# Kernel optimization log

Hardware: AMD Instinct MI355X
Metric: run time of the kernel (lower is better)

Reference implementation:

```python
import jax, jax.numpy as jnp
import numpy as np

DIM = 128
POS_HID = 64
ATT_HID = DIM * 2
B, N = 4, 512


def _linear_init(key, fan_in, fan_out):
    # mimic torch Linear default init scale: U(-1/sqrt(fan_in), 1/sqrt(fan_in))
    kw, kb = jax.random.split(key)
    bound = 1.0 / np.sqrt(fan_in)
    W = jax.random.uniform(kw, (fan_in, fan_out), minval=-bound, maxval=bound, dtype=jnp.float32)
    b = jax.random.uniform(kb, (fan_out,), minval=-bound, maxval=bound, dtype=jnp.float32)
    return W, b


def setup_inputs() -> dict:
    key = jax.random.key(0)
    ks = jax.random.split(key, 6)
    x = jax.random.normal(ks[0], (B, DIM, N), dtype=jnp.float32)
    pos = jax.random.normal(ks[1], (B, N, 3), dtype=jnp.float32)
    Wqkv, bqkv = _linear_init(ks[2], DIM, DIM * 3)
    pW1, pb1 = _linear_init(ks[3], 3, POS_HID)
    pW2, pb2 = _linear_init(ks[4], POS_HID, DIM)
    k5a, k5b = jax.random.split(ks[5])
    aW1, ab1 = _linear_init(k5a, DIM, ATT_HID)
    aW2, ab2 = _linear_init(k5b, ATT_HID, DIM)
    return {"x": x, "pos": pos, "Wqkv": Wqkv, "bqkv": bqkv,
            "pW1": pW1, "pb1": pb1, "pW2": pW2, "pb2": pb2,
            "aW1": aW1, "ab1": ab1, "aW2": aW2, "ab2": ab2}


def reference(x, pos, Wqkv, bqkv, pW1, pb1, pW2, pb2, aW1, ab1, aW2, ab2):
    # x: [b, d, n] -> [b, n, d]
    xt = jnp.transpose(x, (0, 2, 1))
    qkv = xt @ Wqkv + bqkv                      # [b, n, 3d]
    q, k, v = jnp.split(qkv, 3, axis=-1)        # each [b, n, d]

    # pairwise relative positions: [b, i, j, 3]
    rel_pos = pos[:, :, None, :] - pos[:, None, :, :]
    # pos_mlp: Linear(3, hid) -> ReLU -> Linear(hid, d)
    rel_pos_emb = jax.nn.relu(rel_pos @ pW1 + pb1) @ pW2 + pb2   # [b, i, j, d]

    qk_rel = q[:, :, None, :] - k[:, None, :, :]                 # [b, i, j, d]
    v_ij = v[:, None, :, :] + rel_pos_emb                        # [b, i, j, d]

    # attn_mlp: Linear(d, 2d) -> ReLU -> Linear(2d, d)
    sim = jax.nn.relu((qk_rel + rel_pos_emb) @ aW1 + ab1) @ aW2 + ab2  # [b, i, j, d]
    attn = jax.nn.softmax(sim, axis=2)                           # softmax over j (dim=-2)
    agg = jnp.sum(attn * v_ij, axis=2)                           # [b, i, d]
    return jnp.transpose(agg, (0, 2, 1))                         # [b, d, n]
```

## Files before the change

kernel.cpp:

```cpp
#include <hip/hip_runtime.h>
#include <hip/hip_bf16.h>

#define B_ 4
#define N_ 512
#define D_ 128
#define LOG2E 1.4426950408889634f

typedef __attribute__((ext_vector_type(8))) short bf16x8;
typedef __attribute__((ext_vector_type(4))) short s16x4;
typedef __attribute__((ext_vector_type(4))) float f32x4;
typedef __attribute__((ext_vector_type(16))) float f32x16;

__device__ __forceinline__ f32x4 mfma16(bf16x8 a, bf16x8 b, f32x4 c) {
    return __builtin_amdgcn_mfma_f32_16x16x32_bf16(a, b, c, 0, 0, 0);
}
__device__ __forceinline__ f32x16 mfma32(bf16x8 a, bf16x8 b, f32x16 c) {
    return __builtin_amdgcn_mfma_f32_32x32x16_bf16(a, b, c, 0, 0, 0);
}
__device__ __forceinline__ short bf16b(float x) {
    __hip_bfloat16 h = __float2bfloat16(x);
    return *reinterpret_cast<short*>(&h);
}
__device__ __forceinline__ float b2f(short s) {
    unsigned u = ((unsigned)(unsigned short)s) << 16;
    union { unsigned u; float f; } c; c.u = u; return c.f;
}

__global__ void prep_misc_kernel(const float* __restrict__ aW1, const float* __restrict__ aW2,
                                 const float* __restrict__ pW2, const float* __restrict__ pb2,
                                 const float* __restrict__ ab1, const float* __restrict__ pos,
                                 const float* __restrict__ pW1, const float* __restrict__ x,
                                 const float* __restrict__ Wqkv, const float* __restrict__ bqkv,
                                 __hip_bfloat16* __restrict__ aW2T, __hip_bfloat16* __restrict__ pW2T,
                                 __hip_bfloat16* __restrict__ W12T, float* __restrict__ cvec,
                                 float* __restrict__ posw,
                                 float* __restrict__ q, float* __restrict__ k,
                                 short* __restrict__ vb_t) {
    const int bid = blockIdx.x;
    const int tid = threadIdx.x;
    if (bid < 128) {
        int idx = bid * 256 + tid;
        {
            int n = idx >> 8, k2 = idx & 255;
            aW2T[idx] = __float2bfloat16(aW2[k2 * 128 + n] * LOG2E);
        }
        if (idx < 128 * 64) {
            int n = idx >> 6, k2 = idx & 63;
            pW2T[idx] = __float2bfloat16(pW2[k2 * 128 + n]);
        }
        if (idx < 256 * 64) {
            int n = idx >> 6, h = idx & 63;
            float s = 0.f;
#pragma unroll 8
            for (int d = 0; d < 128; ++d) s += pW2[h * 128 + d] * aW1[d * 256 + n];
            W12T[idx] = __float2bfloat16(s);
        }
        if (idx < 256) {
            float s = ab1[idx];
#pragma unroll 8
            for (int d = 0; d < 128; ++d) s += pb2[d] * aW1[d * 256 + idx];
            cvec[idx] = s;
        }
    } else if (bid < 256) {
        int i4 = (bid - 128) * 256 + tid;
        int t = i4 >> 4, h4 = (i4 & 15) * 4;
        float p0 = pos[t * 3 + 0], p1 = pos[t * 3 + 1], p2 = pos[t * 3 + 2];
#pragma unroll
        for (int e = 0; e < 4; ++e) {
            int h = h4 + e;
            posw[t * 64 + h] = p0 * pW1[h] + p1 * pW1[64 + h] + p2 * pW1[128 + h];
        }
    } else {
        int idx = (bid - 256) * 256 + tid;
        int m = idx % 384;
        int g = idx / 384;
        int bn0 = g * 16;
        int b = bn0 >> 9, n0 = bn0 & (N_ - 1);
        const float* xp = x + (b * D_) * N_ + n0;
        float bias = bqkv[m];
        float acc[16];
#pragma unroll
        for (int t = 0; t < 16; ++t) acc[t] = bias;
#pragma unroll 2
        for (int d = 0; d < D_; ++d) {
            float wv = Wqkv[d * 384 + m];
            const float* xr = xp + d * N_;
            float4 x0 = *(const float4*)(xr);
            float4 x1 = *(const float4*)(xr + 4);
            float4 x2 = *(const float4*)(xr + 8);
            float4 x3 = *(const float4*)(xr + 12);
            acc[0]  = fmaf(x0.x, wv, acc[0]);  acc[1]  = fmaf(x0.y, wv, acc[1]);
            acc[2]  = fmaf(x0.z, wv, acc[2]);  acc[3]  = fmaf(x0.w, wv, acc[3]);
            acc[4]  = fmaf(x1.x, wv, acc[4]);  acc[5]  = fmaf(x1.y, wv, acc[5]);
            acc[6]  = fmaf(x1.z, wv, acc[6]);  acc[7]  = fmaf(x1.w, wv, acc[7]);
            acc[8]  = fmaf(x2.x, wv, acc[8]);  acc[9]  = fmaf(x2.y, wv, acc[9]);
            acc[10] = fmaf(x2.z, wv, acc[10]); acc[11] = fmaf(x2.w, wv, acc[11]);
            acc[12] = fmaf(x3.x, wv, acc[12]); acc[13] = fmaf(x3.y, wv, acc[13]);
            acc[14] = fmaf(x3.z, wv, acc[14]); acc[15] = fmaf(x3.w, wv, acc[15]);
        }
        if (m < 256) {
            float* dst = (m < 128) ? q : k;
            int mm = m & 127;
#pragma unroll
            for (int t = 0; t < 16; ++t)
                dst[(bn0 + t) * D_ + mm] = acc[t];
        } else {
            int d = m & 127;
            int jt = n0 >> 6;
            int jr = n0 & 63;
            int rtv = jr >> 5;
            int jrr0 = jr & 31;
            int ct = d >> 5;
            int lbase = d & 31;
            size_t tilebase = (size_t)b * 65536 + (size_t)jt * 8192
                            + (size_t)((rtv * 4 + ct) * 64) * 16;
#pragma unroll
            for (int tt = 0; tt < 4; ++tt) {
                int jrr = jrr0 + tt * 4;
                int rb = 4 * (jrr >> 3);
                int hi = (jrr >> 2) & 1;
                s16x4 pk;
                pk[0] = bf16b(acc[tt * 4 + 0]); pk[1] = bf16b(acc[tt * 4 + 1]);
                pk[2] = bf16b(acc[tt * 4 + 2]); pk[3] = bf16b(acc[tt * 4 + 3]);
                *(s16x4*)(vb_t + tilebase + (size_t)(lbase + 32 * hi) * 16 + rb) = pk;
            }
        }
    }
}

__global__ void qka_kernel(const float* __restrict__ q, const float* __restrict__ k,
                           const float* __restrict__ aW1,
                           float* __restrict__ qa, short* __restrict__ kab_t) {
    int col = threadIdx.x;
    int bn0 = blockIdx.x * 8;
    int b = bn0 >> 9, n0 = bn0 & (N_ - 1);
    const float* qp = q + (size_t)bn0 * D_;
    const float* kp = k + (size_t)bn0 * D_;
    float aq[8], ak[8];
#pragma unroll
    for (int t = 0; t < 8; ++t) { aq[t] = 0.f; ak[t] = 0.f; }
#pragma unroll 2
    for (int d = 0; d < D_; ++d) {
        float wv = aW1[d * 256 + col];
#pragma unroll
        for (int t = 0; t < 8; ++t) {
            aq[t] = fmaf(qp[t * D_ + d], wv, aq[t]);
            ak[t] = fmaf(kp[t * D_ + d], wv, ak[t]);
        }
    }
#pragma unroll
    for (int t = 0; t < 8; ++t)
        qa[(size_t)(bn0 + t) * 256 + col] = aq[t];
    int jt = n0 >> 6;
    int mt = (n0 >> 4) & 3;
    int lg0 = (n0 >> 2) & 3;
    int w = col >> 5, nt = (col >> 4) & 1, lc = col & 15;
#pragma unroll
    for (int half = 0; half < 2; ++half) {
        int lg = lg0 + half;
        int l = lg * 16 + lc;
        s16x4 pk;
        pk[0] = bf16b(ak[half * 4 + 0]); pk[1] = bf16b(ak[half * 4 + 1]);
        pk[2] = bf16b(ak[half * 4 + 2]); pk[3] = bf16b(ak[half * 4 + 3]);
        size_t base = (((((size_t)b * 8 + jt) * 8 + w) * 2 + nt) * 4 + mt) * 256 + l * 4;
        *(s16x4*)(kab_t + base) = pk;
    }
}

__global__ __launch_bounds__(512, 2) void fused_attn_kernel(
    const float* __restrict__ qa, const short* __restrict__ kab_t,
    const short* __restrict__ vb_t,
    const float* __restrict__ posw, const float* __restrict__ pb1,
    const __hip_bfloat16* __restrict__ pW2T, const float* __restrict__ pb2,
    const __hip_bfloat16* __restrict__ W12T, const float* __restrict__ cvec,
    const __hip_bfloat16* __restrict__ aW2T, const float* __restrict__ ab2,
    float* __restrict__ out)
{
    __shared__ __hip_bfloat16 ph_s[2][64][72];
    __shared__ __hip_bfloat16 hid_s[2][64][264];
    __shared__ float pwi_s[2][64];
    __shared__ float mrg_s[2][4][32][4];

    const int tid = threadIdx.x;
    const int w   = tid >> 6;
    const int l   = tid & 63;
    const int lg  = l >> 4;
    const int lc  = l & 15;
    const int l31 = l & 31;
    const int hi  = l >> 5;
    const int rt  = w >> 2;
    const int ct  = w & 3;
    const int gx8 = ((l31 >> 2) & 3) << 3;

    const int blk = (blockIdx.x & 7) * 128 + (blockIdx.x >> 3);
    const int b   = blk >> 8;
    const int i0  = (blk & 255) * 2;

    if (tid < 128) {
        int ii = tid >> 6, h = tid & 63;
        pwi_s[ii][h] = posw[(size_t)(b * N_ + i0 + ii) * 64 + h] + pb1[h];
    }

    const int col0  = 32 * w + lc;
    const int dcol2 = 32 * ct + l31;

    const float qr00 = qa[(b * N_ + i0) * 256 + col0] + cvec[col0];
    const float qr01 = qa[(b * N_ + i0) * 256 + col0 + 16] + cvec[col0 + 16];
    const float qr10 = qa[(b * N_ + i0 + 1) * 256 + col0] + cvec[col0];
    const float qr11 = qa[(b * N_ + i0 + 1) * 256 + col0 + 16] + cvec[col0 + 16];
    const float ab2_r = ab2[dcol2] * LOG2E;
    const float pb2_r = pb2[dcol2];

    const __hip_bfloat16* a2base = aW2T + (size_t)dcol2 * 256 + 8 * hi;
    bf16x8 bw2[16];
#pragma unroll
    for (int ks = 0; ks < 16; ++ks)
        bw2[ks] = *(const bf16x8*)(a2base + 16 * ks);
    const __hip_bfloat16* ppb = pW2T + (size_t)dcol2 * 64 + 8 * hi;
    const __hip_bfloat16* p12b = W12T + (size_t)(32 * w + lc) * 64 + 8 * lg;

    float m_run[2] = {-1e30f, -1e30f};
    float l_run[2] = {0.f, 0.f};
    float o_run[2] = {0.f, 0.f};
    float vv[2][16];

    const short* ktp0 = kab_t + (size_t)b * 131072 + w * 2048 + l * 4;
    const short* vtp0 = vb_t + (size_t)b * 65536 + ((rt * 4 + ct) * 64 + l) * 16;

    const int jl = tid >> 3;
    const int hb = (tid & 7) * 8;

    s16x4 vb4[4], kv[2][4];
#pragma unroll
    for (int q4 = 0; q4 < 4; ++q4)
        vb4[q4] = *(const s16x4*)(vtp0 + 4 * q4);
#pragma unroll
    for (int nt = 0; nt < 2; ++nt)
#pragma unroll
        for (int mt = 0; mt < 4; ++mt)
            kv[nt][mt] = *(const s16x4*)(ktp0 + nt * 1024 + mt * 256);
    __syncthreads();

    for (int jt = 0; jt < 8; ++jt) {
        bf16x8 bwp[4], bw12[2][2];
#pragma unroll
        for (int ks = 0; ks < 4; ++ks)
            bwp[ks] = *(const bf16x8*)(ppb + 16 * ks);
#pragma unroll
        for (int nt = 0; nt < 2; ++nt)
#pragma unroll
            for (int k2 = 0; k2 < 2; ++k2)
                bw12[nt][k2] = *(const bf16x8*)(p12b + nt * 1024 + k2 * 32);

        {
            const float* pj = posw + (size_t)(b * N_ + jt * 64 + jl) * 64 + hb;
            float4 x0 = *(const float4*)pj;
            float4 x1 = *(const float4*)(pj + 4);
            float xr[8] = {x0.x, x0.y, x0.z, x0.w, x1.x, x1.y, x1.z, x1.w};
#pragma unroll
            for (int ii = 0; ii < 2; ++ii) {
                bf16x8 tv;
#pragma unroll
                for (int h = 0; h < 8; ++h)
                    tv[h] = bf16b(fmaxf(pwi_s[ii][hb + h] - xr[h], 0.f));
                *(bf16x8*)(&ph_s[ii][jl][hb]) = tv;
            }
        }
        __syncthreads();

#pragma unroll
        for (int ii = 0; ii < 2; ++ii) {
            f32x16 accr = {0.f,0.f,0.f,0.f,0.f,0.f,0.f,0.f,0.f,0.f,0.f,0.f,0.f,0.f,0.f,0.f};
#pragma unroll
            for (int ks = 0; ks < 4; ++ks) {
                bf16x8 a = *(const bf16x8*)(&ph_s[ii][32 * rt + l31][16 * ks + 8 * hi]);
                accr = mfma32(a, bwp[ks], accr);
            }
#pragma unroll
            for (int r = 0; r < 16; ++r)
                vv[ii][r] = accr[r] + b2f(vb4[r >> 2][r & 3]) + pb2_r;
        }
#pragma unroll
        for (int ii = 0; ii < 2; ++ii) {
#pragma unroll
            for (int mt = 0; mt < 4; ++mt) {
                bf16x8 a0 = *(const bf16x8*)(&ph_s[ii][mt * 16 + lc][8 * lg]);
                bf16x8 a1 = *(const bf16x8*)(&ph_s[ii][mt * 16 + lc][32 + 8 * lg]);
#pragma unroll
                for (int nt = 0; nt < 2; ++nt) {
                    f32x4 acc = {0.f, 0.f, 0.f, 0.f};
                    acc = mfma16(a0, bw12[nt][0], acc);
                    acc = mfma16(a1, bw12[nt][1], acc);
                    const float qv = ii ? (nt ? qr11 : qr10) : (nt ? qr01 : qr00);
                    const int colw = 32 * w + (((16 * nt + lc) ^ (8 * lg)) & 31);
#pragma unroll
                    for (int r = 0; r < 4; ++r) {
                        int row = mt * 16 + 4 * lg + r;
                        hid_s[ii][row][colw] = __float2bfloat16(
                            fmaxf(acc[r] + qv - b2f(kv[nt][mt][r]), 0.f));
                    }
                }
            }
        }
        __syncthreads();

        {
            const int jtn = (jt < 7) ? jt + 1 : 7;
            const short* vtp = vtp0 + (size_t)jtn * 8192;
            const short* ktp = ktp0 + (size_t)jtn * 16384;
#pragma unroll
            for (int q4 = 0; q4 < 4; ++q4)
                vb4[q4] = *(const s16x4*)(vtp + 4 * q4);
#pragma unroll
            for (int nt = 0; nt < 2; ++nt)
#pragma unroll
                for (int mt = 0; mt < 4; ++mt)
                    kv[nt][mt] = *(const s16x4*)(ktp + nt * 1024 + mt * 256);
        }

#pragma unroll
        for (int ii = 0; ii < 2; ++ii) {
            f32x16 acc2a = {0.f,0.f,0.f,0.f,0.f,0.f,0.f,0.f,0.f,0.f,0.f,0.f,0.f,0.f,0.f,0.f};
            f32x16 acc2b = {0.f,0.f,0.f,0.f,0.f,0.f,0.f,0.f,0.f,0.f,0.f,0.f,0.f,0.f,0.f,0.f};
            const short* hrow = (const short*)&hid_s[ii][32 * rt + l31][0];
#pragma unroll
            for (int ks = 0; ks < 8; ++ks) {
                bf16x8 aa = *(const bf16x8*)(hrow + ((16 * ks + 8 * hi) ^ gx8));
                bf16x8 ab = *(const bf16x8*)(hrow + ((16 * (ks + 8) + 8 * hi) ^ gx8));
                acc2a = mfma32(aa, bw2[ks], acc2a);
                acc2b = mfma32(ab, bw2[ks + 8], acc2b);
            }
#pragma unroll
            for (int r = 0; r < 16; ++r) acc2a[r] += acc2b[r];
            float t8[8];
#pragma unroll
            for (int r = 0; r < 8; ++r) t8[r] = fmaxf(acc2a[r], acc2a[r + 8]);
            float t4a = fmaxf(t8[0], t8[4]), t4b = fmaxf(t8[1], t8[5]);
            float t4c = fmaxf(t8[2], t8[6]), t4d = fmaxf(t8[3], t8[7]);
            float tmax = fmaxf(fmaxf(t4a, t4b), fmaxf(t4c, t4d));
            float m_new = fmaxf(m_run[ii], tmax + ab2_r);
            float mm = m_new - ab2_r;
            float scale = __builtin_amdgcn_exp2f(m_run[ii] - m_new);
            l_run[ii] *= scale;
            o_run[ii] *= scale;
#pragma unroll
            for (int r = 0; r < 16; ++r) {
                float e = __builtin_amdgcn_exp2f(acc2a[r] - mm);
                l_run[ii] += e;
                o_run[ii] = fmaf(e, vv[ii][r], o_run[ii]);
            }
            m_run[ii] = m_new;
        }
    }

    float M1[2], L1[2], O1[2];
#pragma unroll
    for (int ii = 0; ii < 2; ++ii) {
        float m2 = __shfl_xor(m_run[ii], 32);
        float l2 = __shfl_xor(l_run[ii], 32);
        float o2 = __shfl_xor(o_run[ii], 32);
        M1[ii] = fmaxf(m_run[ii], m2);
        float e1 = __builtin_amdgcn_exp2f(m_run[ii] - M1[ii]);
        float e2 = __builtin_amdgcn_exp2f(m2 - M1[ii]);
        L1[ii] = l_run[ii] * e1 + l2 * e2;
        O1[ii] = o_run[ii] * e1 + o2 * e2;
        if (rt == 1 && hi == 0) {
            mrg_s[ii][ct][l31][0] = M1[ii];
            mrg_s[ii][ct][l31][1] = L1[ii];
            mrg_s[ii][ct][l31][2] = O1[ii];
        }
    }
    __syncthreads();
    if (rt == 0 && hi == 0) {
#pragma unroll
        for (int ii = 0; ii < 2; ++ii) {
            float Mb = mrg_s[ii][ct][l31][0];
            float Lb = mrg_s[ii][ct][l31][1];
            float Ob = mrg_s[ii][ct][l31][2];
            float M = fmaxf(M1[ii], Mb);
            float ea = __builtin_amdgcn_exp2f(M1[ii] - M);
            float eb = __builtin_amdgcn_exp2f(Mb - M);
            float L = L1[ii] * ea + Lb * eb;
            float O = O1[ii] * ea + Ob * eb;
            out[((size_t)b * D_ + dcol2) * N_ + i0 + ii] = O / L;
        }
    }
}

extern "C" void kernel_launch(void* const* d_in, const int* in_sizes, int n_in,
                              void* d_out, int out_size, void* d_ws, size_t ws_size,
                              hipStream_t stream) {
    const float* x    = (const float*)d_in[0];
    const float* pos  = (const float*)d_in[1];
    const float* Wqkv = (const float*)d_in[2];
    const float* bqkv = (const float*)d_in[3];
    const float* pW1  = (const float*)d_in[4];
    const float* pb1  = (const float*)d_in[5];
    const float* pW2  = (const float*)d_in[6];
    const float* pb2  = (const float*)d_in[7];
    const float* aW1  = (const float*)d_in[8];
    const float* ab1  = (const float*)d_in[9];
    const float* aW2  = (const float*)d_in[10];
    const float* ab2  = (const float*)d_in[11];
    float* out = (float*)d_out;

    float* q    = (float*)d_ws;
    float* k    = q  + B_ * N_ * D_;
    float* qa   = k  + B_ * N_ * D_;
    float* posw = qa + B_ * N_ * 256;
    float* cvec = posw + B_ * N_ * 64;
    short* kab_t = (short*)(cvec + 256);
    short* vb_t  = kab_t + B_ * N_ * 256;
    __hip_bfloat16* aW2T = (__hip_bfloat16*)(vb_t + B_ * N_ * D_);
    __hip_bfloat16* pW2T = aW2T + 128 * 256;
    __hip_bfloat16* W12T = pW2T + 128 * 64;

    hipLaunchKernelGGL(prep_misc_kernel, dim3(448), dim3(256), 0, stream,
                       aW1, aW2, pW2, pb2, ab1, pos, pW1, x, Wqkv, bqkv,
                       aW2T, pW2T, W12T, cvec, posw, q, k, vb_t);
    hipLaunchKernelGGL(qka_kernel, dim3(256), dim3(256), 0, stream,
                       q, k, aW1, qa, kab_t);
    hipLaunchKernelGGL(fused_attn_kernel, dim3(1024), dim3(512), 0, stream,
                       qa, kab_t, vb_t, posw, pb1, pW2T, pb2, W12T, cvec, aW2T, ab2, out);
}
```

Before: 217.5 us.

## Process one query row per 256-thread block with wider per-wave column tiles

The fused attention kernel now handles one query position per block using 4 waves, where it previously handled two positions with 8 waves. Each wave covers 64 hidden columns and two output column tiles. Weights are loaded from global or cache inside the loop instead of being held in registers, and the next position-hidden tile is computed after the softmax step. Launch bounds move to 256 threads with 3 blocks per CU and the grid doubles. The goal is lower register pressure, fewer barriers per block and higher occupancy. The cost is that weights are no longer reused across two query rows and more global weight loads are issued.

```diff
diff --git a/kernel.cpp b/kernel.cpp
--- a/kernel.cpp
+++ b/kernel.cpp
@@ -167,7 +167,7 @@
     }
 }
 
-__global__ __launch_bounds__(512, 2) void fused_attn_kernel(
+__global__ __launch_bounds__(256, 3) void fused_attn_kernel(
     const float* __restrict__ qa, const short* __restrict__ kab_t,
     const short* __restrict__ vb_t,
     const float* __restrict__ posw, const float* __restrict__ pb1,
@@ -176,10 +176,10 @@
     const __hip_bfloat16* __restrict__ aW2T, const float* __restrict__ ab2,
     float* __restrict__ out)
 {
-    __shared__ __hip_bfloat16 ph_s[2][64][72];
-    __shared__ __hip_bfloat16 hid_s[2][64][264];
-    __shared__ float pwi_s[2][64];
-    __shared__ float mrg_s[2][4][32][4];
+    __shared__ __hip_bfloat16 ph_s[64][72];
+    __shared__ __hip_bfloat16 hid_s[64][264];
+    __shared__ float pwi_s[64];
+    __shared__ float mrg_s[2][32][6];
 
     const int tid = threadIdx.x;
     const int w   = tid >> 6;
@@ -188,201 +188,226 @@
     const int lc  = l & 15;
     const int l31 = l & 31;
     const int hi  = l >> 5;
-    const int rt  = w >> 2;
-    const int ct  = w & 3;
+    const int rt  = w >> 1;
+    const int ctw = w & 1;
     const int gx8 = ((l31 >> 2) & 3) << 3;
 
-    const int blk = (blockIdx.x & 7) * 128 + (blockIdx.x >> 3);
-    const int b   = blk >> 8;
-    const int i0  = (blk & 255) * 2;
-
-    if (tid < 128) {
-        int ii = tid >> 6, h = tid & 63;
-        pwi_s[ii][h] = posw[(size_t)(b * N_ + i0 + ii) * 64 + h] + pb1[h];
-    }
-
-    const int col0  = 32 * w + lc;
-    const int dcol2 = 32 * ct + l31;
-
-    const float qr00 = qa[(b * N_ + i0) * 256 + col0] + cvec[col0];
-    const float qr01 = qa[(b * N_ + i0) * 256 + col0 + 16] + cvec[col0 + 16];
-    const float qr10 = qa[(b * N_ + i0 + 1) * 256 + col0] + cvec[col0];
-    const float qr11 = qa[(b * N_ + i0 + 1) * 256 + col0 + 16] + cvec[col0 + 16];
-    const float ab2_r = ab2[dcol2] * LOG2E;
-    const float pb2_r = pb2[dcol2];
-
-    const __hip_bfloat16* a2base = aW2T + (size_t)dcol2 * 256 + 8 * hi;
-    bf16x8 bw2[16];
-#pragma unroll
-    for (int ks = 0; ks < 16; ++ks)
-        bw2[ks] = *(const bf16x8*)(a2base + 16 * ks);
-    const __hip_bfloat16* ppb = pW2T + (size_t)dcol2 * 64 + 8 * hi;
-    const __hip_bfloat16* p12b = W12T + (size_t)(32 * w + lc) * 64 + 8 * lg;
-
-    float m_run[2] = {-1e30f, -1e30f};
-    float l_run[2] = {0.f, 0.f};
-    float o_run[2] = {0.f, 0.f};
-    float vv[2][16];
-
-    const short* ktp0 = kab_t + (size_t)b * 131072 + w * 2048 + l * 4;
-    const short* vtp0 = vb_t + (size_t)b * 65536 + ((rt * 4 + ct) * 64 + l) * 16;
-
-    const int jl = tid >> 3;
-    const int hb = (tid & 7) * 8;
-
-    s16x4 vb4[4], kv[2][4];
-#pragma unroll
-    for (int q4 = 0; q4 < 4; ++q4)
-        vb4[q4] = *(const s16x4*)(vtp0 + 4 * q4);
-#pragma unroll
-    for (int nt = 0; nt < 2; ++nt)
-#pragma unroll
-        for (int mt = 0; mt < 4; ++mt)
-            kv[nt][mt] = *(const s16x4*)(ktp0 + nt * 1024 + mt * 256);
+    const int blk = (blockIdx.x & 7) * 256 + (blockIdx.x >> 3);
+    const int b   = blk >> 9;
+    const int i   = blk & (N_ - 1);
+
+    if (tid < 64) pwi_s[tid] = posw[(size_t)(b * N_ + i) * 64 + tid] + pb1[tid];
+
+    const int col0 = 64 * w + lc;
+    float qr[4];
+#pragma unroll
+    for (int nt = 0; nt < 4; ++nt)
+        qr[nt] = qa[(b * N_ + i) * 256 + col0 + 16 * nt] + cvec[col0 + 16 * nt];
+
+    const int d1 = 64 * ctw + l31;
+    const int d2 = d1 + 32;
+    const float ab2_1 = ab2[d1] * LOG2E, ab2_2 = ab2[d2] * LOG2E;
+    const float pb2_1 = pb2[d1], pb2_2 = pb2[d2];
+
+    const short* ktp0 = kab_t + (size_t)b * 131072 + (2 * w) * 2048 + l * 4;
+    const short* vtp0 = vb_t + (size_t)b * 65536 + (size_t)((rt * 4 + 2 * ctw) * 64 + l) * 16;
+    const __hip_bfloat16* a2b1 = aW2T + (size_t)d1 * 256 + 8 * hi;
+    const __hip_bfloat16* a2b2 = aW2T + (size_t)d2 * 256 + 8 * hi;
+    const __hip_bfloat16* ppb1 = pW2T + (size_t)d1 * 64 + 8 * hi;
+    const __hip_bfloat16* ppb2 = pW2T + (size_t)d2 * 64 + 8 * hi;
+    const __hip_bfloat16* p12b = W12T + (size_t)(64 * w + lc) * 64 + 8 * lg;
+
+    float m_r[2] = {-1e30f, -1e30f};
+    float l_r[2] = {0.f, 0.f};
+    float o_r[2] = {0.f, 0.f};
+    float vv1[16], vv2[16];
+
+    const int jl = tid >> 2;
+    const int hb = (tid & 3) * 16;
+
     __syncthreads();
 
+    {
+        const float* pj = posw + (size_t)(b * N_ + jl) * 64 + hb;
+        float4 x0 = *(const float4*)pj;
+        float4 x1 = *(const float4*)(pj + 4);
+        float4 x2 = *(const float4*)(pj + 8);
+        float4 x3 = *(const float4*)(pj + 12);
+        float xr[16] = {x0.x,x0.y,x0.z,x0.w, x1.x,x1.y,x1.z,x1.w,
+                        x2.x,x2.y,x2.z,x2.w, x3.x,x3.y,x3.z,x3.w};
+        bf16x8 t0, t1;
+#pragma unroll
+        for (int h = 0; h < 8; ++h) {
+            t0[h] = bf16b(fmaxf(pwi_s[hb + h] - xr[h], 0.f));
+            t1[h] = bf16b(fmaxf(pwi_s[hb + 8 + h] - xr[8 + h], 0.f));
+        }
+        *(bf16x8*)(&ph_s[jl][hb]) = t0;
+        *(bf16x8*)(&ph_s[jl][hb + 8]) = t1;
+    }
+    __syncthreads();
+
     for (int jt = 0; jt < 8; ++jt) {
-        bf16x8 bwp[4], bw12[2][2];
-#pragma unroll
-        for (int ks = 0; ks < 4; ++ks)
-            bwp[ks] = *(const bf16x8*)(ppb + 16 * ks);
-#pragma unroll
-        for (int nt = 0; nt < 2; ++nt)
-#pragma unroll
-            for (int k2 = 0; k2 < 2; ++k2)
-                bw12[nt][k2] = *(const bf16x8*)(p12b + nt * 1024 + k2 * 32);
+        const short* ktp = ktp0 + (size_t)jt * 16384;
+        const short* vtp = vtp0 + (size_t)jt * 8192;
+        s16x4 vb4a[4], vb4b[4];
+#pragma unroll
+        for (int q4 = 0; q4 < 4; ++q4) {
+            vb4a[q4] = *(const s16x4*)(vtp + 4 * q4);
+            vb4b[q4] = *(const s16x4*)(vtp + 1024 + 4 * q4);
+        }
+        s16x4 kv[4][4];
+#pragma unroll
+        for (int nt = 0; nt < 4; ++nt)
+#pragma unroll
+            for (int mt = 0; mt < 4; ++mt)
+                kv[nt][mt] = *(const s16x4*)(ktp + nt * 1024 + mt * 256);
 
         {
-            const float* pj = posw + (size_t)(b * N_ + jt * 64 + jl) * 64 + hb;
+            bf16x8 aph[4];
+#pragma unroll
+            for (int ks = 0; ks < 4; ++ks)
+                aph[ks] = *(const bf16x8*)(&ph_s[32 * rt + l31][16 * ks + 8 * hi]);
+            f32x16 ac1 = {0.f,0.f,0.f,0.f,0.f,0.f,0.f,0.f,0.f,0.f,0.f,0.f,0.f,0.f,0.f,0.f};
+            f32x16 ac2 = {0.f,0.f,0.f,0.f,0.f,0.f,0.f,0.f,0.f,0.f,0.f,0.f,0.f,0.f,0.f,0.f};
+#pragma unroll
+            for (int ks = 0; ks < 4; ++ks) {
+                bf16x8 b1 = *(const bf16x8*)(ppb1 + 16 * ks);
+                bf16x8 b2 = *(const bf16x8*)(ppb2 + 16 * ks);
+                ac1 = mfma32(aph[ks], b1, ac1);
+                ac2 = mfma32(aph[ks], b2, ac2);
+            }
+#pragma unroll
+            for (int r = 0; r < 16; ++r) {
+                vv1[r] = ac1[r] + b2f(vb4a[r >> 2][r & 3]) + pb2_1;
+                vv2[r] = ac2[r] + b2f(vb4b[r >> 2][r & 3]) + pb2_2;
+            }
+        }
+
+#pragma unroll
+        for (int mt = 0; mt < 4; ++mt) {
+            bf16x8 a0 = *(const bf16x8*)(&ph_s[mt * 16 + lc][8 * lg]);
+            bf16x8 a1 = *(const bf16x8*)(&ph_s[mt * 16 + lc][32 + 8 * lg]);
+#pragma unroll
+            for (int nt = 0; nt < 4; ++nt) {
+                bf16x8 w0 = *(const bf16x8*)(p12b + nt * 1024);
+                bf16x8 w1 = *(const bf16x8*)(p12b + nt * 1024 + 32);
+                f32x4 acc = {0.f, 0.f, 0.f, 0.f};
+                acc = mfma16(a0, w0, acc);
+                acc = mfma16(a1, w1, acc);
+                const int colw = 64 * w + ((16 * nt + lc) ^ (8 * lg));
+#pragma unroll
+                for (int r = 0; r < 4; ++r) {
+                    int row = mt * 16 + 4 * lg + r;
+                    hid_s[row][colw] = __float2bfloat16(
+                        fmaxf(acc[r] + qr[nt] - b2f(kv[nt][mt][r]), 0.f));
+                }
+            }
+        }
+        __syncthreads();
+
+        f32x16 acca = {0.f,0.f,0.f,0.f,0.f,0.f,0.f,0.f,0.f,0.f,0.f,0.f,0.f,0.f,0.f,0.f};
+        f32x16 accb = {0.f,0.f,0.f,0.f,0.f,0.f,0.f,0.f,0.f,0.f,0.f,0.f,0.f,0.f,0.f,0.f};
+        {
+            const short* hrow = (const short*)&hid_s[32 * rt + l31][0];
+#pragma unroll
+            for (int ks = 0; ks < 16; ++ks) {
+                bf16x8 a = *(const bf16x8*)(hrow + ((16 * ks + 8 * hi) ^ gx8));
+                bf16x8 w1 = *(const bf16x8*)(a2b1 + 16 * ks);
+                bf16x8 w2 = *(const bf16x8*)(a2b2 + 16 * ks);
+                acca = mfma32(a, w1, acca);
+                accb = mfma32(a, w2, accb);
+            }
+        }
+
+        {
+            float t8[8];
+#pragma unroll
+            for (int r = 0; r < 8; ++r) t8[r] = fmaxf(acca[r], acca[r + 8]);
+            float ta = fmaxf(fmaxf(t8[0], t8[4]), fmaxf(t8[1], t8[5]));
+            float tb = fmaxf(fmaxf(t8[2], t8[6]), fmaxf(t8[3], t8[7]));
+            float tmax = fmaxf(ta, tb);
+            float m_new = fmaxf(m_r[0], tmax + ab2_1);
+            float mm = m_new - ab2_1;
+            float scale = __builtin_amdgcn_exp2f(m_r[0] - m_new);
+            l_r[0] *= scale; o_r[0] *= scale;
+#pragma unroll
+            for (int r = 0; r < 16; ++r) {
+                float e = __builtin_amdgcn_exp2f(acca[r] - mm);
+                l_r[0] += e;
+                o_r[0] = fmaf(e, vv1[r], o_r[0]);
+            }
+            m_r[0] = m_new;
+        }
+        {
+            float t8[8];
+#pragma unroll
+            for (int r = 0; r < 8; ++r) t8[r] = fmaxf(accb[r], accb[r + 8]);
+            float ta = fmaxf(fmaxf(t8[0], t8[4]), fmaxf(t8[1], t8[5]));
+            float tb = fmaxf(fmaxf(t8[2], t8[6]), fmaxf(t8[3], t8[7]));
+            float tmax = fmaxf(ta, tb);
+            float m_new = fmaxf(m_r[1], tmax + ab2_2);
+            float mm = m_new - ab2_2;
+            float scale = __builtin_amdgcn_exp2f(m_r[1] - m_new);
+            l_r[1] *= scale; o_r[1] *= scale;
+#pragma unroll
+            for (int r = 0; r < 16; ++r) {
+                float e = __builtin_amdgcn_exp2f(accb[r] - mm);
+                l_r[1] += e;
+                o_r[1] = fmaf(e, vv2[r], o_r[1]);
+            }
+            m_r[1] = m_new;
+        }
+
+        if (jt < 7) {
+            const float* pj = posw + (size_t)(b * N_ + (jt + 1) * 64 + jl) * 64 + hb;
             float4 x0 = *(const float4*)pj;
             float4 x1 = *(const float4*)(pj + 4);
-            float xr[8] = {x0.x, x0.y, x0.z, x0.w, x1.x, x1.y, x1.z, x1.w};
-#pragma unroll
-            for (int ii = 0; ii < 2; ++ii) {
-                bf16x8 tv;
-#pragma unroll
-                for (int h = 0; h < 8; ++h)
-                    tv[h] = bf16b(fmaxf(pwi_s[ii][hb + h] - xr[h], 0.f));
-                *(bf16x8*)(&ph_s[ii][jl][hb]) = tv;
-            }
+            float4 x2 = *(const float4*)(pj + 8);
+            float4 x3 = *(const float4*)(pj + 12);
+            float xr[16] = {x0.x,x0.y,x0.z,x0.w, x1.x,x1.y,x1.z,x1.w,
+                            x2.x,x2.y,x2.z,x2.w, x3.x,x3.y,x3.z,x3.w};
+            bf16x8 t0, t1;
+#pragma unroll
+            for (int h = 0; h < 8; ++h) {
+                t0[h] = bf16b(fmaxf(pwi_s[hb + h] - xr[h], 0.f));
+                t1[h] = bf16b(fmaxf(pwi_s[hb + 8 + h] - xr[8 + h], 0.f));
+            }
+            *(bf16x8*)(&ph_s[jl][hb]) = t0;
+            *(bf16x8*)(&ph_s[jl][hb + 8]) = t1;
         }
         __syncthreads();
-
-#pragma unroll
-        for (int ii = 0; ii < 2; ++ii) {
-            f32x16 accr = {0.f,0.f,0.f,0.f,0.f,0.f,0.f,0.f,0.f,0.f,0.f,0.f,0.f,0.f,0.f,0.f};
-#pragma unroll
-            for (int ks = 0; ks < 4; ++ks) {
-                bf16x8 a = *(const bf16x8*)(&ph_s[ii][32 * rt + l31][16 * ks + 8 * hi]);
-                accr = mfma32(a, bwp[ks], accr);
-            }
-#pragma unroll
-            for (int r = 0; r < 16; ++r)
-                vv[ii][r] = accr[r] + b2f(vb4[r >> 2][r & 3]) + pb2_r;
-        }
-#pragma unroll
-        for (int ii = 0; ii < 2; ++ii) {
-#pragma unroll
-            for (int mt = 0; mt < 4; ++mt) {
-                bf16x8 a0 = *(const bf16x8*)(&ph_s[ii][mt * 16 + lc][8 * lg]);
-                bf16x8 a1 = *(const bf16x8*)(&ph_s[ii][mt * 16 + lc][32 + 8 * lg]);
-#pragma unroll
-                for (int nt = 0; nt < 2; ++nt) {
-                    f32x4 acc = {0.f, 0.f, 0.f, 0.f};
-                    acc = mfma16(a0, bw12[nt][0], acc);
-                    acc = mfma16(a1, bw12[nt][1], acc);
-                    const float qv = ii ? (nt ? qr11 : qr10) : (nt ? qr01 : qr00);
-                    const int colw = 32 * w + (((16 * nt + lc) ^ (8 * lg)) & 31);
-#pragma unroll
-                    for (int r = 0; r < 4; ++r) {
-                        int row = mt * 16 + 4 * lg + r;
-                        hid_s[ii][row][colw] = __float2bfloat16(
-                            fmaxf(acc[r] + qv - b2f(kv[nt][mt][r]), 0.f));
-                    }
-                }
-            }
-        }
-        __syncthreads();
-
-        {
-            const int jtn = (jt < 7) ? jt + 1 : 7;
-            const short* vtp = vtp0 + (size_t)jtn * 8192;
-            const short* ktp = ktp0 + (size_t)jtn * 16384;
-#pragma unroll
-            for (int q4 = 0; q4 < 4; ++q4)
-                vb4[q4] = *(const s16x4*)(vtp + 4 * q4);
-#pragma unroll
-            for (int nt = 0; nt < 2; ++nt)
-#pragma unroll
-                for (int mt = 0; mt < 4; ++mt)
-                    kv[nt][mt] = *(const s16x4*)(ktp + nt * 1024 + mt * 256);
-        }
-
-#pragma unroll
-        for (int ii = 0; ii < 2; ++ii) {
-            f32x16 acc2a = {0.f,0.f,0.f,0.f,0.f,0.f,0.f,0.f,0.f,0.f,0.f,0.f,0.f,0.f,0.f,0.f};
-            f32x16 acc2b = {0.f,0.f,0.f,0.f,0.f,0.f,0.f,0.f,0.f,0.f,0.f,0.f,0.f,0.f,0.f,0.f};
-            const short* hrow = (const short*)&hid_s[ii][32 * rt + l31][0];
-#pragma unroll
-            for (int ks = 0; ks < 8; ++ks) {
-                bf16x8 aa = *(const bf16x8*)(hrow + ((16 * ks + 8 * hi) ^ gx8));
-                bf16x8 ab = *(const bf16x8*)(hrow + ((16 * (ks + 8) + 8 * hi) ^ gx8));
-                acc2a = mfma32(aa, bw2[ks], acc2a);
-                acc2b = mfma32(ab, bw2[ks + 8], acc2b);
-            }
-#pragma unroll
-            for (int r = 0; r < 16; ++r) acc2a[r] += acc2b[r];
-            float t8[8];
-#pragma unroll
-            for (int r = 0; r < 8; ++r) t8[r] = fmaxf(acc2a[r], acc2a[r + 8]);
-            float t4a = fmaxf(t8[0], t8[4]), t4b = fmaxf(t8[1], t8[5]);
-            float t4c = fmaxf(t8[2], t8[6]), t4d = fmaxf(t8[3], t8[7]);
-            float tmax = fmaxf(fmaxf(t4a, t4b), fmaxf(t4c, t4d));
-            float m_new = fmaxf(m_run[ii], tmax + ab2_r);
-            float mm = m_new - ab2_r;
-            float scale = __builtin_amdgcn_exp2f(m_run[ii] - m_new);
-            l_run[ii] *= scale;
-            o_run[ii] *= scale;
-#pragma unroll
-            for (int r = 0; r < 16; ++r) {
-                float e = __builtin_amdgcn_exp2f(acc2a[r] - mm);
-                l_run[ii] += e;
-                o_run[ii] = fmaf(e, vv[ii][r], o_run[ii]);
-            }
-            m_run[ii] = m_new;
-        }
-    }
-
-    float M1[2], L1[2], O1[2];
-#pragma unroll
-    for (int ii = 0; ii < 2; ++ii) {
-        float m2 = __shfl_xor(m_run[ii], 32);
-        float l2 = __shfl_xor(l_run[ii], 32);
-        float o2 = __shfl_xor(o_run[ii], 32);
-        M1[ii] = fmaxf(m_run[ii], m2);
-        float e1 = __builtin_amdgcn_exp2f(m_run[ii] - M1[ii]);
-        float e2 = __builtin_amdgcn_exp2f(m2 - M1[ii]);
-        L1[ii] = l_run[ii] * e1 + l2 * e2;
-        O1[ii] = o_run[ii] * e1 + o2 * e2;
-        if (rt == 1 && hi == 0) {
-            mrg_s[ii][ct][l31][0] = M1[ii];
-            mrg_s[ii][ct][l31][1] = L1[ii];
-            mrg_s[ii][ct][l31][2] = O1[ii];
-        }
+    }
+
+    float M[2], L[2], O[2];
+#pragma unroll
+    for (int c = 0; c < 2; ++c) {
+        float mo = __shfl_xor(m_r[c], 32);
+        float lo = __shfl_xor(l_r[c], 32);
+        float oo = __shfl_xor(o_r[c], 32);
+        M[c] = fmaxf(m_r[c], mo);
+        float e1 = __builtin_amdgcn_exp2f(m_r[c] - M[c]);
+        float e2 = __builtin_amdgcn_exp2f(mo - M[c]);
+        L[c] = l_r[c] * e1 + lo * e2;
+        O[c] = o_r[c] * e1 + oo * e2;
+    }
+    if (rt == 1 && hi == 0) {
+        mrg_s[ctw][l31][0] = M[0]; mrg_s[ctw][l31][1] = L[0]; mrg_s[ctw][l31][2] = O[0];
+        mrg_s[ctw][l31][3] = M[1]; mrg_s[ctw][l31][4] = L[1]; mrg_s[ctw][l31][5] = O[1];
     }
     __syncthreads();
     if (rt == 0 && hi == 0) {
 #pragma unroll
-        for (int ii = 0; ii < 2; ++ii) {
-            float Mb = mrg_s[ii][ct][l31][0];
-            float Lb = mrg_s[ii][ct][l31][1];
-            float Ob = mrg_s[ii][ct][l31][2];
-            float M = fmaxf(M1[ii], Mb);
-            float ea = __builtin_amdgcn_exp2f(M1[ii] - M);
-            float eb = __builtin_amdgcn_exp2f(Mb - M);
-            float L = L1[ii] * ea + Lb * eb;
-            float O = O1[ii] * ea + Ob * eb;
-            out[((size_t)b * D_ + dcol2) * N_ + i0 + ii] = O / L;
+        for (int c = 0; c < 2; ++c) {
+            float Mb = mrg_s[ctw][l31][3 * c + 0];
+            float Lb = mrg_s[ctw][l31][3 * c + 1];
+            float Ob = mrg_s[ctw][l31][3 * c + 2];
+            float Mf = fmaxf(M[c], Mb);
+            float ea = __builtin_amdgcn_exp2f(M[c] - Mf);
+            float eb = __builtin_amdgcn_exp2f(Mb - Mf);
+            float Lf = L[c] * ea + Lb * eb;
+            float Of = O[c] * ea + Ob * eb;
+            int d = (c == 0) ? d1 : d2;
+            out[((size_t)b * D_ + d) * N_ + i] = Of / Lf;
         }
     }
 }
@@ -420,6 +445,6 @@
                        aW2T, pW2T, W12T, cvec, posw, q, k, vb_t);
     hipLaunchKernelGGL(qka_kernel, dim3(256), dim3(256), 0, stream,
                        q, k, aW1, qa, kab_t);
-    hipLaunchKernelGGL(fused_attn_kernel, dim3(1024), dim3(512), 0, stream,
+    hipLaunchKernelGGL(fused_attn_kernel, dim3(2048), dim3(256), 0, stream,
                        qa, kab_t, vb_t, posw, pb1, pW2T, pb2, W12T, cvec, aW2T, ab2, out);
 }
```

After: 657.0 us. +202.2%, slower.

## Transpose hidden-layer MFMA to write packed hid_s rows and fold pb2 into V

Applied to the files above, without the earlier changes.

Swaps the MFMA operand order in the first attention-MLP layer so each lane produces four consecutive hidden columns for one j row. This lets it write a packed 4-element bf16 vector into shared memory with a new XOR swizzle instead of four scalar stores. The kab_t layout and the q-row register loads are reshaped to match the new accumulator mapping. The pb2 bias is now added once when V is written rather than per tile inside the attention loop. The new kab_t layout uses scattered scalar stores in the small producer kernel, and the swizzle has to stay consistent with the existing gx8 read pattern.

```diff
diff --git a/kernel.cpp b/kernel.cpp
--- a/kernel.cpp
+++ b/kernel.cpp
@@ -106,6 +106,7 @@
                 dst[(bn0 + t) * D_ + mm] = acc[t];
         } else {
             int d = m & 127;
+            float pv = pb2[d];
             int jt = n0 >> 6;
             int jr = n0 & 63;
             int rtv = jr >> 5;
@@ -120,8 +121,8 @@
                 int rb = 4 * (jrr >> 3);
                 int hi = (jrr >> 2) & 1;
                 s16x4 pk;
-                pk[0] = bf16b(acc[tt * 4 + 0]); pk[1] = bf16b(acc[tt * 4 + 1]);
-                pk[2] = bf16b(acc[tt * 4 + 2]); pk[3] = bf16b(acc[tt * 4 + 3]);
+                pk[0] = bf16b(acc[tt * 4 + 0] + pv); pk[1] = bf16b(acc[tt * 4 + 1] + pv);
+                pk[2] = bf16b(acc[tt * 4 + 2] + pv); pk[3] = bf16b(acc[tt * 4 + 3] + pv);
                 *(s16x4*)(vb_t + tilebase + (size_t)(lbase + 32 * hi) * 16 + rb) = pk;
             }
         }
@@ -151,19 +152,16 @@
 #pragma unroll
     for (int t = 0; t < 8; ++t)
         qa[(size_t)(bn0 + t) * 256 + col] = aq[t];
-    int jt = n0 >> 6;
-    int mt = (n0 >> 4) & 3;
-    int lg0 = (n0 >> 2) & 3;
-    int w = col >> 5, nt = (col >> 4) & 1, lc = col & 15;
-#pragma unroll
-    for (int half = 0; half < 2; ++half) {
-        int lg = lg0 + half;
-        int l = lg * 16 + lc;
-        s16x4 pk;
-        pk[0] = bf16b(ak[half * 4 + 0]); pk[1] = bf16b(ak[half * 4 + 1]);
-        pk[2] = bf16b(ak[half * 4 + 2]); pk[3] = bf16b(ak[half * 4 + 3]);
-        size_t base = (((((size_t)b * 8 + jt) * 8 + w) * 2 + nt) * 4 + mt) * 256 + l * 4;
-        *(s16x4*)(kab_t + base) = pk;
+    int jtK = n0 >> 6;
+    int w = col >> 5, t4 = (col >> 4) & 1, lgn = (col >> 2) & 3, rn = col & 3;
+#pragma unroll
+    for (int tok = 0; tok < 8; ++tok) {
+        int j = n0 + tok;
+        int jtile = (j >> 4) & 3;
+        int lcj = j & 15;
+        size_t idx = (((((size_t)b * 8 + jtK) * 8 + w) * 2 + t4) * 4 + jtile) * 256
+                   + (size_t)(lgn * 16 + lcj) * 4 + rn;
+        kab_t[idx] = bf16b(ak[tok]);
     }
 }
 
@@ -191,6 +189,7 @@
     const int rt  = w >> 2;
     const int ct  = w & 3;
     const int gx8 = ((l31 >> 2) & 3) << 3;
+    const int sxor = 8 * ((lc >> 2) & 3);
 
     const int blk = (blockIdx.x & 7) * 128 + (blockIdx.x >> 3);
     const int b   = blk >> 8;
@@ -201,15 +200,25 @@
         pwi_s[ii][h] = posw[(size_t)(b * N_ + i0 + ii) * 64 + h] + pb1[h];
     }
 
-    const int col0  = 32 * w + lc;
     const int dcol2 = 32 * ct + l31;
 
-    const float qr00 = qa[(b * N_ + i0) * 256 + col0] + cvec[col0];
-    const float qr01 = qa[(b * N_ + i0) * 256 + col0 + 16] + cvec[col0 + 16];
-    const float qr10 = qa[(b * N_ + i0 + 1) * 256 + col0] + cvec[col0];
-    const float qr11 = qa[(b * N_ + i0 + 1) * 256 + col0 + 16] + cvec[col0 + 16];
+    float qr[2][2][4];
+    {
+        const int nb = 32 * w + 4 * lg;
+        float4 cv0 = *(const float4*)(cvec + nb);
+        float4 cv1 = *(const float4*)(cvec + nb + 16);
+#pragma unroll
+        for (int ii = 0; ii < 2; ++ii) {
+            const float* qp = qa + (size_t)(b * N_ + i0 + ii) * 256 + nb;
+            float4 q0 = *(const float4*)qp;
+            float4 q1 = *(const float4*)(qp + 16);
+            qr[ii][0][0] = q0.x + cv0.x; qr[ii][0][1] = q0.y + cv0.y;
+            qr[ii][0][2] = q0.z + cv0.z; qr[ii][0][3] = q0.w + cv0.w;
+            qr[ii][1][0] = q1.x + cv1.x; qr[ii][1][1] = q1.y + cv1.y;
+            qr[ii][1][2] = q1.z + cv1.z; qr[ii][1][3] = q1.w + cv1.w;
+        }
+    }
     const float ab2_r = ab2[dcol2] * LOG2E;
-    const float pb2_r = pb2[dcol2];
 
     const __hip_bfloat16* a2base = aW2T + (size_t)dcol2 * 256 + 8 * hi;
     bf16x8 bw2[16];
@@ -235,10 +244,10 @@
     for (int q4 = 0; q4 < 4; ++q4)
         vb4[q4] = *(const s16x4*)(vtp0 + 4 * q4);
 #pragma unroll
-    for (int nt = 0; nt < 2; ++nt)
-#pragma unroll
-        for (int mt = 0; mt < 4; ++mt)
-            kv[nt][mt] = *(const s16x4*)(ktp0 + nt * 1024 + mt * 256);
+    for (int t = 0; t < 2; ++t)
+#pragma unroll
+        for (int jt2 = 0; jt2 < 4; ++jt2)
+            kv[t][jt2] = *(const s16x4*)(ktp0 + t * 1024 + jt2 * 256);
     __syncthreads();
 
     for (int jt = 0; jt < 8; ++jt) {
@@ -247,10 +256,10 @@
         for (int ks = 0; ks < 4; ++ks)
             bwp[ks] = *(const bf16x8*)(ppb + 16 * ks);
 #pragma unroll
-        for (int nt = 0; nt < 2; ++nt)
+        for (int t = 0; t < 2; ++t)
 #pragma unroll
             for (int k2 = 0; k2 < 2; ++k2)
-                bw12[nt][k2] = *(const bf16x8*)(p12b + nt * 1024 + k2 * 32);
+                bw12[t][k2] = *(const bf16x8*)(p12b + t * 1024 + k2 * 32);
 
         {
             const float* pj = posw + (size_t)(b * N_ + jt * 64 + jl) * 64 + hb;
@@ -278,27 +287,25 @@
             }
 #pragma unroll
             for (int r = 0; r < 16; ++r)
-                vv[ii][r] = accr[r] + b2f(vb4[r >> 2][r & 3]) + pb2_r;
+                vv[ii][r] = accr[r] + b2f(vb4[r >> 2][r & 3]);
         }
 #pragma unroll
         for (int ii = 0; ii < 2; ++ii) {
 #pragma unroll
-            for (int mt = 0; mt < 4; ++mt) {
-                bf16x8 a0 = *(const bf16x8*)(&ph_s[ii][mt * 16 + lc][8 * lg]);
-                bf16x8 a1 = *(const bf16x8*)(&ph_s[ii][mt * 16 + lc][32 + 8 * lg]);
-#pragma unroll
-                for (int nt = 0; nt < 2; ++nt) {
+            for (int jt2 = 0; jt2 < 4; ++jt2) {
+                bf16x8 a0 = *(const bf16x8*)(&ph_s[ii][jt2 * 16 + lc][8 * lg]);
+                bf16x8 a1 = *(const bf16x8*)(&ph_s[ii][jt2 * 16 + lc][32 + 8 * lg]);
+#pragma unroll
+                for (int t = 0; t < 2; ++t) {
                     f32x4 acc = {0.f, 0.f, 0.f, 0.f};
-                    acc = mfma16(a0, bw12[nt][0], acc);
-                    acc = mfma16(a1, bw12[nt][1], acc);
-                    const float qv = ii ? (nt ? qr11 : qr10) : (nt ? qr01 : qr00);
-                    const int colw = 32 * w + (((16 * nt + lc) ^ (8 * lg)) & 31);
-#pragma unroll
-                    for (int r = 0; r < 4; ++r) {
-                        int row = mt * 16 + 4 * lg + r;
-                        hid_s[ii][row][colw] = __float2bfloat16(
-                            fmaxf(acc[r] + qv - b2f(kv[nt][mt][r]), 0.f));
-                    }
+                    acc = mfma16(bw12[t][0], a0, acc);
+                    acc = mfma16(bw12[t][1], a1, acc);
+                    s16x4 pk;
+#pragma unroll
+                    for (int r = 0; r < 4; ++r)
+                        pk[r] = bf16b(fmaxf(acc[r] + qr[ii][t][r] - b2f(kv[t][jt2][r]), 0.f));
+                    const int nsw = 32 * w + ((16 * t + 4 * lg) ^ sxor);
+                    *(s16x4*)(&hid_s[ii][jt2 * 16 + lc][nsw]) = pk;
                 }
             }
         }
@@ -312,10 +319,10 @@
             for (int q4 = 0; q4 < 4; ++q4)
                 vb4[q4] = *(const s16x4*)(vtp + 4 * q4);
 #pragma unroll
-            for (int nt = 0; nt < 2; ++nt)
-#pragma unroll
-                for (int mt = 0; mt < 4; ++mt)
-                    kv[nt][mt] = *(const s16x4*)(ktp + nt * 1024 + mt * 256);
+            for (int t = 0; t < 2; ++t)
+#pragma unroll
+                for (int jt2 = 0; jt2 < 4; ++jt2)
+                    kv[t][jt2] = *(const s16x4*)(ktp + t * 1024 + jt2 * 256);
         }
 
 #pragma unroll
```

After: 215.7 us. No clear change (-0.8%).
